# Kernel optimization log

Hardware: AMD Instinct MI355X
Metric: run time of the kernel (lower is better)

## Reference

```python
import jax, jax.numpy as jnp
import numpy as np

N_NODES = 50000
N_EDGES = 800000
IN_CH = 128
OUT_CH = 64
HEADS = 4
NEG_SLOPE = 0.2


def gat_layer(x, src, dst, W, a_src, a_dst, b, n):
    """One GATConv (PyG semantics, self-loops already in src/dst).
    x:[n,Fin], W:[Fin,H*C], a_src/a_dst:[H,C], b:[H*C]. Returns [n,H*C] (concat heads)."""
    H, C = a_src.shape
    h = (x @ W).reshape(n, H, C)                      # [n,H,C]
    alpha_s = jnp.einsum('nhc,hc->nh', h, a_src)      # [n,H]
    alpha_d = jnp.einsum('nhc,hc->nh', h, a_dst)
    e = jax.nn.leaky_relu(alpha_s[src] + alpha_d[dst], NEG_SLOPE)  # [E,H]
    m = jax.ops.segment_max(e, dst, num_segments=n)   # per-dst-node max (stable softmax)
    p = jnp.exp(e - m[dst])
    denom = jax.ops.segment_sum(p, dst, num_segments=n)
    alpha = p / (denom[dst] + 1e-16)                  # [E,H]
    out = jax.ops.segment_sum(h[src] * alpha[:, :, None], dst, num_segments=n)
    return out.reshape(n, H * C) + b


def setup_inputs() -> dict:
    key = jax.random.key(0)
    ks = jax.random.split(key, 10)
    x = jax.random.normal(ks[0], (N_NODES, IN_CH), dtype=jnp.float32)
    edge_index = jax.random.randint(ks[1], (2, N_EDGES), 0, N_NODES, dtype=jnp.int64)
    s = 0.05
    W1 = jax.random.normal(ks[2], (IN_CH, HEADS * OUT_CH), dtype=jnp.float32) * s
    a_src1 = jax.random.normal(ks[3], (HEADS, OUT_CH), dtype=jnp.float32) * s
    a_dst1 = jax.random.normal(ks[4], (HEADS, OUT_CH), dtype=jnp.float32) * s
    b1 = jnp.zeros((HEADS * OUT_CH,), dtype=jnp.float32)
    W2 = jax.random.normal(ks[5], (HEADS * OUT_CH, OUT_CH), dtype=jnp.float32) * s
    a_src2 = jax.random.normal(ks[6], (1, OUT_CH), dtype=jnp.float32) * s
    a_dst2 = jax.random.normal(ks[7], (1, OUT_CH), dtype=jnp.float32) * s
    b2 = jnp.zeros((OUT_CH,), dtype=jnp.float32)
    return {"x": x, "edge_index": edge_index, "W1": W1, "a_src1": a_src1,
            "a_dst1": a_dst1, "b1": b1, "W2": W2, "a_src2": a_src2,
            "a_dst2": a_dst2, "b2": b2}


def reference(x, edge_index, W1, a_src1, a_dst1, b1, W2, a_src2, a_dst2, b2):
    n = x.shape[0]
    # PyG GATConv adds self-loops by default
    loops = jnp.arange(n, dtype=edge_index.dtype)
    src = jnp.concatenate([edge_index[0], loops])
    dst = jnp.concatenate([edge_index[1], loops])
    h = jax.nn.relu(gat_layer(x, src, dst, W1, a_src1, a_dst1, b1, n))
    return gat_layer(h, src, dst, W2, a_src2, a_dst2, b2, n)
```

## Files before the change

kernel.cpp:

```cpp
#include <hip/hip_runtime.h>
#include <math.h>

#define N_NODES   50000
#define E0_EDGES  800000
#define E_TOT     (E0_EDGES + N_NODES)
#define FIN       128
#define F1        256
#define H1        4
#define C2        64
#define NEG_SLOPE 0.2f

typedef short bf16x8 __attribute__((ext_vector_type(8)));
typedef float f32x4  __attribute__((ext_vector_type(4)));

__device__ __forceinline__ unsigned short f2bf(float f) {
  unsigned u = __float_as_uint(f);
  u = (u + 0x7FFFu + ((u >> 16) & 1u)) >> 16;
  return (unsigned short)u;
}
__device__ __forceinline__ float bf2f(unsigned short h) {
  return __uint_as_float((unsigned)h << 16);
}
__device__ __forceinline__ float leaky(float v) {
  return v >= 0.f ? v : NEG_SLOPE * v;
}

__global__ __launch_bounds__(256) void deg_kernel(
    const int* __restrict__ ei, int* __restrict__ count) {
  int e = blockIdx.x * 256 + threadIdx.x;
  if (e >= E_TOT) return;
  int dst = (e < E0_EDGES) ? ei[E0_EDGES + e] : (e - E0_EDGES);
  atomicAdd(&count[dst], 1);
}

__global__ __launch_bounds__(256) void scanA_kernel(
    const int* __restrict__ cnt, int* __restrict__ bsum, int n) {
  int i = blockIdx.x * 256 + threadIdx.x;
  int v = (i < n) ? cnt[i] : 0;
#pragma unroll
  for (int d = 1; d < 64; d <<= 1) v += __shfl_xor(v, d);
  __shared__ int ws[4];
  if ((threadIdx.x & 63) == 0) ws[threadIdx.x >> 6] = v;
  __syncthreads();
  if (threadIdx.x == 0) bsum[blockIdx.x] = ws[0] + ws[1] + ws[2] + ws[3];
}

__global__ __launch_bounds__(256) void scanB_kernel(
    const int* __restrict__ bsum, int* __restrict__ bexcl,
    int* __restrict__ off_n, int nb) {
  const int t = threadIdx.x, lane = t & 63, wid = t >> 6;
  int v = (t < nb) ? bsum[t] : 0;
  int sv = v;
#pragma unroll
  for (int d = 1; d < 64; d <<= 1) {
    int u = __shfl_up(sv, d);
    if (lane >= d) sv += u;
  }
  __shared__ int ws[4];
  if (lane == 63) ws[wid] = sv;
  __syncthreads();
  int add = 0;
  for (int k = 0; k < wid; ++k) add += ws[k];
  int incl = sv + add;
  if (t < nb) bexcl[t] = incl - v;
  if (t == 255) off_n[0] = incl;
}

__global__ __launch_bounds__(256) void scanC_kernel(
    const int* __restrict__ cnt, const int* __restrict__ bexcl,
    int* __restrict__ off, int n) {
  const int t = threadIdx.x, lane = t & 63, wid = t >> 6;
  int i = blockIdx.x * 256 + t;
  int v = (i < n) ? cnt[i] : 0;
  int sv = v;
#pragma unroll
  for (int d = 1; d < 64; d <<= 1) {
    int u = __shfl_up(sv, d);
    if (lane >= d) sv += u;
  }
  __shared__ int ws[4];
  if (lane == 63) ws[wid] = sv;
  __syncthreads();
  int add = 0;
  for (int k = 0; k < wid; ++k) add += ws[k];
  if (i < n) off[i] = sv + add - v + bexcl[blockIdx.x];
}

__global__ __launch_bounds__(256) void scatter_kernel(
    const int* __restrict__ ei, const int* __restrict__ offset,
    int* __restrict__ cursor, int* __restrict__ csr_src) {
  int e = blockIdx.x * 256 + threadIdx.x;
  if (e >= E_TOT) return;
  int src, dst;
  if (e < E0_EDGES) { src = ei[e]; dst = ei[E0_EDGES + e]; }
  else              { src = e - E0_EDGES; dst = src; }
  int pos = offset[dst] + atomicAdd(&cursor[dst], 1);
  csr_src[pos] = src;
}

__global__ __launch_bounds__(256) void gemm1_kernel(
    const float* __restrict__ A, const float* __restrict__ B,
    unsigned short* __restrict__ C, float* __restrict__ as1,
    float* __restrict__ ad1, const float* __restrict__ a_s,
    const float* __restrict__ a_d, int M) {
  constexpr int K = FIN, BN = 128, KP = K + 8, NF = BN / 16;
  __shared__ unsigned short BT[BN * KP];
  const int tid = threadIdx.x, lane = tid & 63, wid = tid >> 6;
  const int gy = blockIdx.y, n0 = gy * BN;

  for (int idx = tid; idx < K * (BN / 8); idx += 256) {
    int k = idx >> 4;
    int c = idx & 15;
    const float* src = &B[(size_t)k * F1 + n0 + c * 8];
    float4 lo = *reinterpret_cast<const float4*>(src);
    float4 hi = *reinterpret_cast<const float4*>(src + 4);
    int nb = c * 8;
    BT[(nb + 0) * KP + k] = f2bf(lo.x); BT[(nb + 1) * KP + k] = f2bf(lo.y);
    BT[(nb + 2) * KP + k] = f2bf(lo.z); BT[(nb + 3) * KP + k] = f2bf(lo.w);
    BT[(nb + 4) * KP + k] = f2bf(hi.x); BT[(nb + 5) * KP + k] = f2bf(hi.y);
    BT[(nb + 6) * KP + k] = f2bf(hi.z); BT[(nb + 7) * KP + k] = f2bf(hi.w);
  }
  __syncthreads();

  const int r0 = (blockIdx.x * 4 + wid) * 16;
  if (r0 >= M) return;
  const int nlane = lane & 15;
  const int kg    = (lane >> 4) * 8;
  const int arow  = min(r0 + nlane, M - 1);

  f32x4 acc[NF];
#pragma unroll
  for (int nf = 0; nf < NF; ++nf) acc[nf] = (f32x4){0.f, 0.f, 0.f, 0.f};

  const float* ap = &A[(size_t)arow * K + kg];
#pragma unroll
  for (int kk = 0; kk < K; kk += 32) {
    float4 v0 = *reinterpret_cast<const float4*>(ap + kk);
    float4 v1 = *reinterpret_cast<const float4*>(ap + kk + 4);
    bf16x8 a;
    a[0] = (short)f2bf(v0.x); a[1] = (short)f2bf(v0.y);
    a[2] = (short)f2bf(v0.z); a[3] = (short)f2bf(v0.w);
    a[4] = (short)f2bf(v1.x); a[5] = (short)f2bf(v1.y);
    a[6] = (short)f2bf(v1.z); a[7] = (short)f2bf(v1.w);
#pragma unroll
    for (int nf = 0; nf < NF; ++nf) {
      bf16x8 b = *reinterpret_cast<const bf16x8*>(&BT[(nf * 16 + nlane) * KP + kk + kg]);
      acc[nf] = __builtin_amdgcn_mfma_f32_16x16x32_bf16(a, b, acc[nf], 0, 0, 0);
    }
  }

  const int crow = r0 + (lane >> 4) * 4;
#pragma unroll
  for (int nf = 0; nf < NF; ++nf) {
    const int cc = n0 + nf * 16 + nlane;
#pragma unroll
    for (int j = 0; j < 4; ++j) {
      int rr = crow + j;
      if (rr < M) C[(size_t)rr * F1 + cc] = f2bf(acc[nf][j]);
    }
  }

#pragma unroll
  for (int j = 0; j < 4; ++j) {
    float ps0 = 0.f, ps1 = 0.f, pd0 = 0.f, pd1 = 0.f;
#pragma unroll
    for (int nf = 0; nf < NF; ++nf) {
      int col = n0 + nf * 16 + nlane;
      float v = acc[nf][j];
      float sc = a_s[col], dc = a_d[col];
      if (nf < 4) { ps0 = fmaf(v, sc, ps0); pd0 = fmaf(v, dc, pd0); }
      else        { ps1 = fmaf(v, sc, ps1); pd1 = fmaf(v, dc, pd1); }
    }
#pragma unroll
    for (int d = 1; d < 16; d <<= 1) {
      ps0 += __shfl_xor(ps0, d); ps1 += __shfl_xor(ps1, d);
      pd0 += __shfl_xor(pd0, d); pd1 += __shfl_xor(pd1, d);
    }
    int row = crow + j;
    if (nlane == 0 && row < M) {
      float2 s2 = {ps0, ps1}, d2 = {pd0, pd1};
      *reinterpret_cast<float2*>(&as1[row * 4 + gy * 2]) = s2;
      *reinterpret_cast<float2*>(&ad1[row * 4 + gy * 2]) = d2;
    }
  }
}

__global__ __launch_bounds__(256) void gemm2_kernel(
    const unsigned short* __restrict__ A, const float* __restrict__ B,
    unsigned short* __restrict__ C, float* __restrict__ as2,
    float* __restrict__ ad2, const float* __restrict__ a_s,
    const float* __restrict__ a_d, int M) {
  constexpr int K = F1, BN = 64, KP = K + 8, NF = BN / 16;
  __shared__ unsigned short BT[BN * KP];
  const int tid = threadIdx.x, lane = tid & 63, wid = tid >> 6;

  for (int idx = tid; idx < K * (BN / 8); idx += 256) {
    int k = idx >> 3;
    int c = idx & 7;
    const float* src = &B[(size_t)k * C2 + c * 8];
    float4 lo = *reinterpret_cast<const float4*>(src);
    float4 hi = *reinterpret_cast<const float4*>(src + 4);
    int nb = c * 8;
    BT[(nb + 0) * KP + k] = f2bf(lo.x); BT[(nb + 1) * KP + k] = f2bf(lo.y);
    BT[(nb + 2) * KP + k] = f2bf(lo.z); BT[(nb + 3) * KP + k] = f2bf(lo.w);
    BT[(nb + 4) * KP + k] = f2bf(hi.x); BT[(nb + 5) * KP + k] = f2bf(hi.y);
    BT[(nb + 6) * KP + k] = f2bf(hi.z); BT[(nb + 7) * KP + k] = f2bf(hi.w);
  }
  __syncthreads();

  const int r0 = (blockIdx.x * 4 + wid) * 16;
  if (r0 >= M) return;
  const int nlane = lane & 15;
  const int kg    = (lane >> 4) * 8;
  const int arow  = min(r0 + nlane, M - 1);

  f32x4 acc[NF];
#pragma unroll
  for (int nf = 0; nf < NF; ++nf) acc[nf] = (f32x4){0.f, 0.f, 0.f, 0.f};

  const unsigned short* ap = &A[(size_t)arow * K + kg];
#pragma unroll
  for (int kk = 0; kk < K; kk += 32) {
    bf16x8 a = *reinterpret_cast<const bf16x8*>(ap + kk);
#pragma unroll
    for (int nf = 0; nf < NF; ++nf) {
      bf16x8 b = *reinterpret_cast<const bf16x8*>(&BT[(nf * 16 + nlane) * KP + kk + kg]);
      acc[nf] = __builtin_amdgcn_mfma_f32_16x16x32_bf16(a, b, acc[nf], 0, 0, 0);
    }
  }

  const int crow = r0 + (lane >> 4) * 4;
#pragma unroll
  for (int nf = 0; nf < NF; ++nf) {
    const int cc = nf * 16 + nlane;
#pragma unroll
    for (int j = 0; j < 4; ++j) {
      int rr = crow + j;
      if (rr < M) C[(size_t)rr * C2 + cc] = f2bf(acc[nf][j]);
    }
  }

#pragma unroll
  for (int j = 0; j < 4; ++j) {
    float ps = 0.f, pd = 0.f;
#pragma unroll
    for (int nf = 0; nf < NF; ++nf) {
      int col = nf * 16 + nlane;
      float v = acc[nf][j];
      ps = fmaf(v, a_s[col], ps);
      pd = fmaf(v, a_d[col], pd);
    }
#pragma unroll
    for (int d = 1; d < 16; d <<= 1) {
      ps += __shfl_xor(ps, d);
      pd += __shfl_xor(pd, d);
    }
    int row = crow + j;
    if (nlane == 0 && row < M) { as2[row] = ps; ad2[row] = pd; }
  }
}

__global__ __launch_bounds__(256) void aggregate1_kernel(
    const unsigned short* __restrict__ h1b, const float* __restrict__ as,
    const float* __restrict__ ad, const int* __restrict__ csr_src,
    const int* __restrict__ offset, const float* __restrict__ b1,
    unsigned short* __restrict__ out1b, int n) {
  const int lane = threadIdx.x & 63;
  const int node = blockIdx.x * 4 + (threadIdx.x >> 6);
  if (node >= n) return;
  const int beg = offset[node], end = offset[node + 1];
  const int hl = lane >> 4;
  const float adh = ad[node * H1 + hl];
  const unsigned loff = (unsigned)(lane * 4);

  float4 acc = make_float4(0.f, 0.f, 0.f, 0.f);
  float den = 0.f;
  int e = beg;
  for (; e + 7 < end; e += 8) {
    int s[8];
    ushort4 r[8];
    float a[8];
#pragma unroll
    for (int i = 0; i < 8; ++i) s[i] = csr_src[e + i];
#pragma unroll
    for (int i = 0; i < 8; ++i)
      r[i] = *reinterpret_cast<const ushort4*>(h1b + (unsigned)(s[i] * F1) + loff);
#pragma unroll
    for (int i = 0; i < 8; ++i) a[i] = as[s[i] * H1 + hl];
#pragma unroll
    for (int i = 0; i < 8; ++i) {
      const float w = __expf(leaky(a[i] + adh));
      den += w;
      acc.x = fmaf(w, bf2f(r[i].x), acc.x);
      acc.y = fmaf(w, bf2f(r[i].y), acc.y);
      acc.z = fmaf(w, bf2f(r[i].z), acc.z);
      acc.w = fmaf(w, bf2f(r[i].w), acc.w);
    }
  }
  for (; e < end; ++e) {
    const int s0 = csr_src[e];
    const float w = __expf(leaky(as[s0 * H1 + hl] + adh));
    den += w;
    const ushort4 r0 = *reinterpret_cast<const ushort4*>(h1b + (unsigned)(s0 * F1) + loff);
    acc.x = fmaf(w, bf2f(r0.x), acc.x);
    acc.y = fmaf(w, bf2f(r0.y), acc.y);
    acc.z = fmaf(w, bf2f(r0.z), acc.z);
    acc.w = fmaf(w, bf2f(r0.w), acc.w);
  }
  const float inv = 1.f / (den + 1e-16f);
  const float4 bb = *reinterpret_cast<const float4*>(&b1[lane * 4]);
  ushort4 ob;
  ob.x = f2bf(fmaxf(fmaf(acc.x, inv, bb.x), 0.f));
  ob.y = f2bf(fmaxf(fmaf(acc.y, inv, bb.y), 0.f));
  ob.z = f2bf(fmaxf(fmaf(acc.z, inv, bb.z), 0.f));
  ob.w = f2bf(fmaxf(fmaf(acc.w, inv, bb.w), 0.f));
  *reinterpret_cast<ushort4*>(&out1b[(size_t)node * F1 + lane * 4]) = ob;
}

__global__ __launch_bounds__(256) void aggregate2_kernel(
    const unsigned short* __restrict__ h2b, const float* __restrict__ as,
    const float* __restrict__ ad, const int* __restrict__ csr_src,
    const int* __restrict__ offset, const float* __restrict__ b2,
    float* __restrict__ out, int n) {
  const int lane = threadIdx.x & 63;
  const int node = blockIdx.x * 4 + (threadIdx.x >> 6);
  if (node >= n) return;
  const int beg = offset[node], end = offset[node + 1];
  const float adv = ad[node];

  float acc = 0.f;
  float den = 0.f;
  int e = beg;
  for (; e + 7 < end; e += 8) {
    int s[8];
    unsigned short r[8];
    float a[8];
#pragma unroll
    for (int i = 0; i < 8; ++i) s[i] = csr_src[e + i];
#pragma unroll
    for (int i = 0; i < 8; ++i) r[i] = h2b[(unsigned)(s[i] * C2) + lane];
#pragma unroll
    for (int i = 0; i < 8; ++i) a[i] = as[s[i]];
#pragma unroll
    for (int i = 0; i < 8; ++i) {
      const float w = __expf(leaky(a[i] + adv));
      den += w;
      acc = fmaf(w, bf2f(r[i]), acc);
    }
  }
  for (; e < end; ++e) {
    const int s0 = csr_src[e];
    const float w = __expf(leaky(as[s0] + adv));
    den += w;
    acc = fmaf(w, bf2f(h2b[(unsigned)(s0 * C2) + lane]), acc);
  }
  out[(size_t)node * C2 + lane] = fmaf(acc, 1.f / (den + 1e-16f), b2[lane]);
}

extern "C" void kernel_launch(void* const* d_in, const int* in_sizes, int n_in,
                              void* d_out, int out_size, void* d_ws, size_t ws_size,
                              hipStream_t stream) {
  const float* x      = (const float*)d_in[0];
  const int*   ei     = (const int*)d_in[1];
  const float* W1     = (const float*)d_in[2];
  const float* a_src1 = (const float*)d_in[3];
  const float* a_dst1 = (const float*)d_in[4];
  const float* b1     = (const float*)d_in[5];
  const float* W2     = (const float*)d_in[6];
  const float* a_src2 = (const float*)d_in[7];
  const float* a_dst2 = (const float*)d_in[8];
  const float* b2     = (const float*)d_in[9];
  float*       out    = (float*)d_out;

  const int n = N_NODES;
  const int nchunks = (n + 255) / 256;

  char* w = (char*)d_ws;
  unsigned short* h1b   = (unsigned short*)w; w += (size_t)n * F1 * 2;
  unsigned short* out1b = (unsigned short*)w; w += (size_t)n * F1 * 2;
  float*          as1   = (float*)w;          w += (size_t)n * H1 * 4;
  float*          ad1   = (float*)w;          w += (size_t)n * H1 * 4;
  float*          as2   = (float*)w;          w += 200192;
  float*          ad2   = (float*)w;          w += 200192;
  int*            cnt   = (int*)w;            w += 200192;
  int*            cur   = (int*)w;            w += 200192;
  int*            off   = (int*)w;            w += 200704;
  int*            bsum  = (int*)w;            w += 1024;
  int*            bexcl = (int*)w;            w += 1024;
  int*            csr   = (int*)w;            w += 3400192;
  unsigned short* h2b   = h1b;

  hipMemsetAsync(cnt, 0, 2 * 200192, stream);
  deg_kernel<<<(E_TOT + 255) / 256, 256, 0, stream>>>(ei, cnt);
  scanA_kernel<<<nchunks, 256, 0, stream>>>(cnt, bsum, n);
  scanB_kernel<<<1, 256, 0, stream>>>(bsum, bexcl, &off[n], nchunks);
  scanC_kernel<<<nchunks, 256, 0, stream>>>(cnt, bexcl, off, n);
  scatter_kernel<<<(E_TOT + 255) / 256, 256, 0, stream>>>(ei, off, cur, csr);

  {
    dim3 grid((n + 63) / 64, 2);
    gemm1_kernel<<<grid, 256, 0, stream>>>(x, W1, h1b, as1, ad1, a_src1, a_dst1, n);
  }
  aggregate1_kernel<<<(n + 3) / 4, 256, 0, stream>>>(h1b, as1, ad1, csr, off, b1, out1b, n);

  {
    dim3 grid((n + 63) / 64, 1);
    gemm2_kernel<<<grid, 256, 0, stream>>>(out1b, W2, h2b, as2, ad2, a_src2, a_dst2, n);
  }
  aggregate2_kernel<<<(n + 3) / 4, 256, 0, stream>>>(h2b, as2, ad2, csr, off, b2, out, n);
}
```

Baseline: 328.9 us.

## Precompute layer-1 edge attention weights in CSR scatter after GEMM1

The CSR scatter kernel now runs after GEMM1 and also computes the four per-head exp(leaky(as+ad)) edge weights, writing them in CSR order into a new per-edge buffer. The layer-1 aggregation then reads each weight directly instead of gathering alpha_src per edge and evaluating exp per lane. This removes redundant exp work and random gathers of as1 in aggregation, but adds a 13.6 MB write plus a reread, and the scatter's float4 writes land at random positions. The aggregation launch is also split into two halves, which appears to serve no speed purpose.

```diff
diff --git a/kernel.cpp b/kernel.cpp
--- a/kernel.cpp
+++ b/kernel.cpp
@@ -86,9 +86,11 @@
   if (i < n) off[i] = sv + add - v + bexcl[blockIdx.x];
 }
 
-__global__ __launch_bounds__(256) void scatter_kernel(
+__global__ __launch_bounds__(256) void scatter_w_kernel(
     const int* __restrict__ ei, const int* __restrict__ offset,
-    int* __restrict__ cursor, int* __restrict__ csr_src) {
+    int* __restrict__ cursor, int* __restrict__ csr_src,
+    const float* __restrict__ as1, const float* __restrict__ ad1,
+    float* __restrict__ w4) {
   int e = blockIdx.x * 256 + threadIdx.x;
   if (e >= E_TOT) return;
   int src, dst;
@@ -96,6 +98,14 @@
   else              { src = e - E0_EDGES; dst = src; }
   int pos = offset[dst] + atomicAdd(&cursor[dst], 1);
   csr_src[pos] = src;
+  const float4 s4 = *reinterpret_cast<const float4*>(&as1[src * H1]);
+  const float4 d4 = *reinterpret_cast<const float4*>(&ad1[dst * H1]);
+  float4 w;
+  w.x = __expf(leaky(s4.x + d4.x));
+  w.y = __expf(leaky(s4.y + d4.y));
+  w.z = __expf(leaky(s4.z + d4.z));
+  w.w = __expf(leaky(s4.w + d4.w));
+  *reinterpret_cast<float4*>(&w4[(size_t)pos * 4]) = w;
 }
 
 __global__ __launch_bounds__(256) void gemm1_kernel(
@@ -261,16 +271,15 @@
 }
 
 __global__ __launch_bounds__(256) void aggregate1_kernel(
-    const unsigned short* __restrict__ h1b, const float* __restrict__ as,
-    const float* __restrict__ ad, const int* __restrict__ csr_src,
-    const int* __restrict__ offset, const float* __restrict__ b1,
-    unsigned short* __restrict__ out1b, int n) {
+    const unsigned short* __restrict__ h1b, const float* __restrict__ w4,
+    const int* __restrict__ csr_src, const int* __restrict__ offset,
+    const float* __restrict__ b1, unsigned short* __restrict__ out1b,
+    int node0, int n) {
   const int lane = threadIdx.x & 63;
-  const int node = blockIdx.x * 4 + (threadIdx.x >> 6);
+  const int node = node0 + blockIdx.x * 4 + (threadIdx.x >> 6);
   if (node >= n) return;
   const int beg = offset[node], end = offset[node + 1];
   const int hl = lane >> 4;
-  const float adh = ad[node * H1 + hl];
   const unsigned loff = (unsigned)(lane * 4);
 
   float4 acc = make_float4(0.f, 0.f, 0.f, 0.f);
@@ -278,28 +287,27 @@
   int e = beg;
   for (; e + 7 < end; e += 8) {
     int s[8];
+    float wv[8];
     ushort4 r[8];
-    float a[8];
 #pragma unroll
     for (int i = 0; i < 8; ++i) s[i] = csr_src[e + i];
+#pragma unroll
+    for (int i = 0; i < 8; ++i) wv[i] = w4[(size_t)(e + i) * 4 + hl];
 #pragma unroll
     for (int i = 0; i < 8; ++i)
       r[i] = *reinterpret_cast<const ushort4*>(h1b + (unsigned)(s[i] * F1) + loff);
 #pragma unroll
-    for (int i = 0; i < 8; ++i) a[i] = as[s[i] * H1 + hl];
-#pragma unroll
     for (int i = 0; i < 8; ++i) {
-      const float w = __expf(leaky(a[i] + adh));
-      den += w;
-      acc.x = fmaf(w, bf2f(r[i].x), acc.x);
-      acc.y = fmaf(w, bf2f(r[i].y), acc.y);
-      acc.z = fmaf(w, bf2f(r[i].z), acc.z);
-      acc.w = fmaf(w, bf2f(r[i].w), acc.w);
+      den += wv[i];
+      acc.x = fmaf(wv[i], bf2f(r[i].x), acc.x);
+      acc.y = fmaf(wv[i], bf2f(r[i].y), acc.y);
+      acc.z = fmaf(wv[i], bf2f(r[i].z), acc.z);
+      acc.w = fmaf(wv[i], bf2f(r[i].w), acc.w);
     }
   }
   for (; e < end; ++e) {
     const int s0 = csr_src[e];
-    const float w = __expf(leaky(as[s0 * H1 + hl] + adh));
+    const float w = w4[(size_t)e * 4 + hl];
     den += w;
     const ushort4 r0 = *reinterpret_cast<const ushort4*>(h1b + (unsigned)(s0 * F1) + loff);
     acc.x = fmaf(w, bf2f(r0.x), acc.x);
@@ -378,6 +386,7 @@
   char* w = (char*)d_ws;
   unsigned short* h1b   = (unsigned short*)w; w += (size_t)n * F1 * 2;
   unsigned short* out1b = (unsigned short*)w; w += (size_t)n * F1 * 2;
+  float*          w4    = (float*)w;          w += (size_t)E_TOT * 4 * 4;
   float*          as1   = (float*)w;          w += (size_t)n * H1 * 4;
   float*          ad1   = (float*)w;          w += (size_t)n * H1 * 4;
   float*          as2   = (float*)w;          w += 200192;
@@ -395,13 +404,22 @@
   scanA_kernel<<<nchunks, 256, 0, stream>>>(cnt, bsum, n);
   scanB_kernel<<<1, 256, 0, stream>>>(bsum, bexcl, &off[n], nchunks);
   scanC_kernel<<<nchunks, 256, 0, stream>>>(cnt, bexcl, off, n);
-  scatter_kernel<<<(E_TOT + 255) / 256, 256, 0, stream>>>(ei, off, cur, csr);
 
   {
     dim3 grid((n + 63) / 64, 2);
     gemm1_kernel<<<grid, 256, 0, stream>>>(x, W1, h1b, as1, ad1, a_src1, a_dst1, n);
   }
-  aggregate1_kernel<<<(n + 3) / 4, 256, 0, stream>>>(h1b, as1, ad1, csr, off, b1, out1b, n);
+
+  scatter_w_kernel<<<(E_TOT + 255) / 256, 256, 0, stream>>>(
+      ei, off, cur, csr, as1, ad1, w4);
+
+  {
+    const int half = 25000;
+    aggregate1_kernel<<<(half + 3) / 4, 256, 0, stream>>>(
+        h1b, w4, csr, off, b1, out1b, 0, half);
+    aggregate1_kernel<<<(n - half + 3) / 4, 256, 0, stream>>>(
+        h1b, w4, csr, off, b1, out1b, half, n);
+  }
 
   {
     dim3 grid((n + 63) / 64, 1);
```

New measurement: 333.6 us. No clear change (+1.4%).
